# Kernel tuning notes

Hardware: AMD Instinct MI355X
Metric: run time of the kernel (lower is better)

The kernel has to match this reference:

```python
import jax, jax.numpy as jnp
import numpy as np

N_NODES = 100000
N_EDGES = 1600000
IN_C, HID_C, OUT_C, N_CLS = 64, 128, 64, 20


def setup_inputs() -> dict:
    key = jax.random.key(0)
    ks = jax.random.split(key, 8)
    s = lambda k, sh: jax.random.normal(k, sh, dtype=jnp.float32) * (1.0 / np.sqrt(sh[0]))
    return {
        "x": jax.random.normal(ks[0], (N_NODES, IN_C), dtype=jnp.float32),
        "edge_index": jax.random.randint(ks[1], (2, N_EDGES), 0, N_NODES, dtype=jnp.int64),
        "w_self1": s(ks[2], (IN_C, HID_C)),
        "w_neigh1": s(ks[3], (IN_C, HID_C)),
        "b1": jnp.zeros((HID_C,), dtype=jnp.float32),
        "w_self2": s(ks[4], (HID_C, OUT_C)),
        "w_neigh2": s(ks[5], (HID_C, OUT_C)),
        "b2": jnp.zeros((OUT_C,), dtype=jnp.float32),
        "wc": s(ks[6], (OUT_C, N_CLS)),
        "bc": jnp.zeros((N_CLS,), dtype=jnp.float32),
    }


def _sage_mean(feat, src, dst, deg_inv, w_self, w_neigh, b):
    # gather messages along edges, segment-sum at destinations, mean-normalize
    msg_sum = jax.ops.segment_sum(feat[src], dst, num_segments=N_NODES)  # [N, d]
    h_neigh = msg_sum * deg_inv[:, None]
    return feat @ w_self + h_neigh @ w_neigh + b


def reference(x, edge_index, w_self1, w_neigh1, b1, w_self2, w_neigh2, b2, wc, bc):
    src, dst = edge_index[0], edge_index[1]
    deg = jax.ops.segment_sum(jnp.ones((src.shape[0],), dtype=x.dtype), dst,
                              num_segments=N_NODES)
    deg_inv = 1.0 / jnp.maximum(deg, 1.0)  # zero-degree nodes -> 0 neighbor mean
    h = jax.nn.relu(_sage_mean(x, src, dst, deg_inv, w_self1, w_neigh1, b1))
    h = jax.nn.relu(_sage_mean(h, src, dst, deg_inv, w_self2, w_neigh2, b2))
    return h @ wc + bc
```

## Files before the change

### kernel.cpp

```cpp
#include <hip/hip_runtime.h>

#define N_NODES 100000
#define N_EDGES 1600000
#define IN_C    64
#define HID_C   128
#define OUT_C   64
#define N_CLS   20

#define BUCKETS 196
#define XSL     8
#define WCAP    2560
#define EPB     4096
#define CAPB    44

#define EB2       391
#define CVT_BLOCKS 3125
#define NTILES    3125
#define MLP_GRID  512

typedef __attribute__((ext_vector_type(8))) short short8;
typedef __attribute__((ext_vector_type(4))) float floatx4;

__device__ __forceinline__ unsigned short f2bf(float f) {
    union { float f; unsigned u; } v; v.f = f;
    unsigned r = v.u + 0x7FFFu + ((v.u >> 16) & 1u);
    return (unsigned short)(r >> 16);
}
__device__ __forceinline__ unsigned pk2(float lo, float hi) {
    return (unsigned)f2bf(lo) | ((unsigned)f2bf(hi) << 16);
}
__device__ __forceinline__ float bflo(unsigned w) { return __uint_as_float(w << 16); }
__device__ __forceinline__ float bfhi(unsigned w) { return __uint_as_float(w & 0xFFFF0000u); }

#define ACC8(v) do { \
    a0 += bflo((v).x); a1 += bfhi((v).x); a2 += bflo((v).y); a3 += bfhi((v).y); \
    a4 += bflo((v).z); a5 += bfhi((v).z); a6 += bflo((v).w); a7 += bfhi((v).w); } while (0)

__global__ __launch_bounds__(256) void binA_kernel(
        const int* __restrict__ ei, int* __restrict__ bcnt,
        unsigned* __restrict__ bins,
        const float* __restrict__ x, unsigned short* __restrict__ xb,
        const float* __restrict__ ws1, const float* __restrict__ wn1,
        const float* __restrict__ ws2, const float* __restrict__ wn2,
        unsigned short* __restrict__ wt1s, unsigned short* __restrict__ wt1n,
        unsigned short* __restrict__ wt2s, unsigned short* __restrict__ wt2n)
{
    __shared__ unsigned lbins[BUCKETS * CAPB];
    __shared__ unsigned comp[EPB];
    __shared__ unsigned dsti[EPB];
    __shared__ int lcnt[BUCKETS], lofs[BUCKETS], gb[BUCKETS];
    __shared__ int sd[256];

    const int bid = blockIdx.x;
    const int tid = threadIdx.x;

    if (bid >= EB2) {
        if (bid < EB2 + CVT_BLOCKS) {
            int i = (bid - EB2) * 256 + tid;
            float4 a = ((const float4*)x)[(size_t)i * 2];
            float4 b = ((const float4*)x)[(size_t)i * 2 + 1];
            uint4 r;
            r.x = pk2(a.x, a.y); r.y = pk2(a.z, a.w);
            r.z = pk2(b.x, b.y); r.w = pk2(b.z, b.w);
            ((uint4*)xb)[i] = r;
        } else {
            int i = (bid - EB2 - CVT_BLOCKS) * 256 + tid;
            if (i < 8192) {
                int o = i >> 6, c = i & 63;
                wt1s[i] = f2bf(ws1[c * 128 + o]);
                wt1n[i] = f2bf(wn1[c * 128 + o]);
            } else if (i < 16384) {
                int j = i - 8192;
                int o = j >> 7, c = j & 127;
                wt2s[j] = f2bf(ws2[c * 64 + o]);
                wt2n[j] = f2bf(wn2[c * 64 + o]);
            }
        }
        return;
    }

    const int xcd = bid & (XSL - 1);
    const int e0  = bid * EPB;

    for (int w = tid; w < BUCKETS; w += 256) lcnt[w] = 0;
    __syncthreads();

    for (int it = 0; it < EPB / 256; ++it) {
        int e = e0 + it * 256 + tid;
        if (e >= N_EDGES) break;
        int src = ei[e];
        int dst = ei[N_EDGES + e];
        int b = dst >> 9;
        unsigned pk = ((unsigned)(dst & 511) << 17) | (unsigned)src;
        int pos = atomicAdd(&lcnt[b], 1);
        if (pos < CAPB) {
            lbins[b * CAPB + pos] = pk;
        } else {
            int gp = atomicAdd(&bcnt[b * XSL + xcd], 1);
            if (gp < WCAP)
                bins[(unsigned)(b * XSL + xcd) * WCAP + gp] = pk;
        }
    }
    __syncthreads();

    int c = (tid < BUCKETS) ? min(lcnt[tid], CAPB) : 0;
    sd[tid] = c;
    __syncthreads();
    for (int off = 1; off < 256; off <<= 1) {
        int v = 0;
        if (tid >= off) v = sd[tid - off];
        __syncthreads();
        if (tid >= off) sd[tid] += v;
        __syncthreads();
    }
    if (tid < BUCKETS) lofs[tid] = sd[tid] - c;
    __syncthreads();
    const int T = sd[255];

    if (tid < BUCKETS) {
        int cw = min(lcnt[tid], CAPB);
        gb[tid] = (cw > 0) ? atomicAdd(&bcnt[tid * XSL + xcd], cw) : 0;
    }
    __syncthreads();

    if (tid < BUCKETS) {
        int cw = min(lcnt[tid], CAPB);
        int lo = lofs[tid];
        unsigned wb = (unsigned)(tid * XSL + xcd) * WCAP + (unsigned)gb[tid];
        for (int i = 0; i < cw; ++i) {
            comp[lo + i] = lbins[tid * CAPB + i];
            dsti[lo + i] = wb + i;
        }
    }
    __syncthreads();

    for (int i = tid; i < T; i += 256)
        bins[dsti[i]] = comp[i];
}

__global__ __launch_bounds__(256) void buildB_kernel(
        const int* __restrict__ bcnt, const unsigned* __restrict__ bins,
        int* __restrict__ row_ptr, int* __restrict__ sorted_src,
        float* __restrict__ dinv)
{
    __shared__ unsigned ent[16384];
    __shared__ int scnt[XSL], soff[XSL];
    __shared__ int cnt[512], lofs[512], cur[512];
    __shared__ int sd[256];
    __shared__ int gbase_s;

    const int b   = blockIdx.x;
    const int tid = threadIdx.x;
    const int node0 = b * 512;

    int part = 0;
    for (int w = tid; w < b * XSL; w += 256) part += min(bcnt[w], WCAP);
    sd[tid] = part;
    __syncthreads();
    for (int off = 128; off > 0; off >>= 1) {
        if (tid < off) sd[tid] += sd[tid + off];
        __syncthreads();
    }
    if (tid == 0) {
        gbase_s = sd[0];
        if (b == 0) row_ptr[N_NODES] = N_EDGES;
    }
    __syncthreads();

    if (tid < XSL) scnt[tid] = min(bcnt[b * XSL + tid], WCAP);
    { int i = tid; cnt[i] = 0; cnt[i + 256] = 0; }
    __syncthreads();
    if (tid == 0) {
        int acc = 0;
        for (int sl = 0; sl < XSL; ++sl) {
            soff[sl] = acc;
            acc += scnt[sl];
            if (acc > 16384) { scnt[sl] -= (acc - 16384); acc = 16384; }
        }
    }
    __syncthreads();

    for (int sl = 0; sl < XSL; ++sl) {
        int len = scnt[sl];
        const unsigned* seg = bins + (unsigned)(b * XSL + sl) * WCAP;
        int base = soff[sl];
        for (int i = tid; i < len; i += 256) {
            unsigned e = seg[i];
            ent[base + i] = e;
            atomicAdd((unsigned*)&cnt[e >> 17], 1u);
        }
    }
    __syncthreads();
    const int T = soff[XSL - 1] + scnt[XSL - 1];

    int a0 = cnt[2 * tid], a1 = cnt[2 * tid + 1];
    int s2 = a0 + a1;
    sd[tid] = s2;
    __syncthreads();
    for (int off = 1; off < 256; off <<= 1) {
        int v = 0;
        if (tid >= off) v = sd[tid - off];
        __syncthreads();
        if (tid >= off) sd[tid] += v;
        __syncthreads();
    }
    int excl = sd[tid] - s2;
    lofs[2 * tid]     = excl;
    lofs[2 * tid + 1] = excl + a0;
    cur[2 * tid]      = excl;
    cur[2 * tid + 1]  = excl + a0;
    __syncthreads();

    const int gbase = gbase_s;
    for (int j = tid; j < 512; j += 256) {
        int node = node0 + j;
        if (node < N_NODES) {
            row_ptr[node] = gbase + lofs[j];
            dinv[node] = 1.0f / (float)max(cnt[j], 1);
        }
    }
    for (int i = tid; i < T; i += 256) {
        unsigned e = ent[i];
        int dl = e >> 17;
        int p = atomicAdd((unsigned*)&cur[dl], 1u);
        sorted_src[gbase + p] = (int)(e & 0x1FFFFu);
    }
}

__global__ __launch_bounds__(256) void gather1_kernel(
        const int* __restrict__ row_ptr, const int* __restrict__ srcs,
        const unsigned short* __restrict__ featb,
        const float* __restrict__ dinv, unsigned short* __restrict__ aggb)
{
    int gid = blockIdx.x * 256 + threadIdx.x;
    int n = gid >> 3;
    int q = gid & 7;
    const uint4* f4 = (const uint4*)featb;
    float a0=0,a1=0,a2=0,a3=0,a4=0,a5=0,a6=0,a7=0;
    int beg = row_ptr[n];
    int end = row_ptr[n + 1];
    int e = beg;
    for (; e + 4 <= end; e += 4) {
        int s0 = srcs[e], s1 = srcs[e+1], s2 = srcs[e+2], s3 = srcs[e+3];
        uint4 v0 = f4[(size_t)s0 * 8 + q];
        uint4 v1 = f4[(size_t)s1 * 8 + q];
        uint4 v2 = f4[(size_t)s2 * 8 + q];
        uint4 v3 = f4[(size_t)s3 * 8 + q];
        ACC8(v0); ACC8(v1); ACC8(v2); ACC8(v3);
    }
    for (; e < end; ++e) {
        uint4 v = f4[(size_t)srcs[e] * 8 + q];
        ACC8(v);
    }
    float di = dinv[n];
    uint4 r;
    r.x = pk2(a0 * di, a1 * di);
    r.y = pk2(a2 * di, a3 * di);
    r.z = pk2(a4 * di, a5 * di);
    r.w = pk2(a6 * di, a7 * di);
    ((uint4*)aggb)[(size_t)n * 8 + q] = r;
}

__global__ __launch_bounds__(256, 2) void mlp1_kernel(
        const unsigned short* __restrict__ xb,
        const unsigned short* __restrict__ aggb,
        const unsigned short* __restrict__ wt1s,
        const unsigned short* __restrict__ wt1n,
        const float* __restrict__ b1,
        const unsigned short* __restrict__ wt2n,
        const unsigned short* __restrict__ wt2s,
        const float* __restrict__ b2,
        unsigned short* __restrict__ t2b,
        unsigned short* __restrict__ s2b)
{
    __shared__ unsigned short sbuf[32 * 136];

    const int tid  = threadIdx.x;
    const int lane = tid & 63;
    const int wv   = tid >> 6;
    const int quad = lane >> 4;
    const int col  = lane & 15;
    const int nrow = (wv & 1) * 16 + col;
    const int mhalf = wv >> 1;

    short8 wBs0[4], wBs1[4], wBn0[4], wBn1[4];
#pragma unroll
    for (int mt = 0; mt < 4; ++mt) {
        size_t m = (size_t)((mhalf * 4 + mt) * 16 + col);
        wBs0[mt] = *(const short8*)(wt1s + m * 64 +      quad * 8);
        wBs1[mt] = *(const short8*)(wt1s + m * 64 + 32 + quad * 8);
        wBn0[mt] = *(const short8*)(wt1n + m * 64 +      quad * 8);
        wBn1[mt] = *(const short8*)(wt1n + m * 64 + 32 + quad * 8);
    }
    short8 wCt[2][4], wCs[2][4];
#pragma unroll
    for (int mt = 0; mt < 2; ++mt) {
        size_t m = (size_t)((mhalf * 2 + mt) * 16 + col);
#pragma unroll
        for (int kc = 0; kc < 4; ++kc) {
            wCt[mt][kc] = *(const short8*)(wt2n + m * 128 + kc * 32 + quad * 8);
            wCs[mt][kc] = *(const short8*)(wt2s + m * 128 + kc * 32 + quad * 8);
        }
    }
    float4 bv1[4];
#pragma unroll
    for (int mt = 0; mt < 4; ++mt)
        bv1[mt] = *(const float4*)(b1 + (mhalf * 4 + mt) * 16 + quad * 4);
    float4 bv2[2];
#pragma unroll
    for (int mt = 0; mt < 2; ++mt)
        bv2[mt] = *(const float4*)(b2 + (mhalf * 2 + mt) * 16 + quad * 4);

    int tile = blockIdx.x;
    short8 bs0, bs1, bn0, bn1;
    {
        const int nl = tile * 32 + nrow;
        bs0 = *(const short8*)(xb   + (size_t)nl * 64 +      quad * 8);
        bs1 = *(const short8*)(xb   + (size_t)nl * 64 + 32 + quad * 8);
        bn0 = *(const short8*)(aggb + (size_t)nl * 64 +      quad * 8);
        bn1 = *(const short8*)(aggb + (size_t)nl * 64 + 32 + quad * 8);
    }

    while (tile < NTILES) {
        const int nl = tile * 32 + nrow;
        const int next = tile + MLP_GRID;

        floatx4 accB[4];
#pragma unroll
        for (int mt = 0; mt < 4; ++mt) {
            floatx4 acc = {0.f, 0.f, 0.f, 0.f};
            acc = __builtin_amdgcn_mfma_f32_16x16x32_bf16(wBs0[mt], bs0, acc, 0, 0, 0);
            acc = __builtin_amdgcn_mfma_f32_16x16x32_bf16(wBs1[mt], bs1, acc, 0, 0, 0);
            acc = __builtin_amdgcn_mfma_f32_16x16x32_bf16(wBn0[mt], bn0, acc, 0, 0, 0);
            acc = __builtin_amdgcn_mfma_f32_16x16x32_bf16(wBn1[mt], bn1, acc, 0, 0, 0);
            accB[mt] = acc;
        }

        if (next < NTILES) {
            const int nn = next * 32 + nrow;
            bs0 = *(const short8*)(xb   + (size_t)nn * 64 +      quad * 8);
            bs1 = *(const short8*)(xb   + (size_t)nn * 64 + 32 + quad * 8);
            bn0 = *(const short8*)(aggb + (size_t)nn * 64 +      quad * 8);
            bn1 = *(const short8*)(aggb + (size_t)nn * 64 + 32 + quad * 8);
        }

        __syncthreads();
#pragma unroll
        for (int mt = 0; mt < 4; ++mt) {
            int och = (mhalf * 4 + mt) * 16 + quad * 4;
            ushort4 r;
            r.x = f2bf(fmaxf(accB[mt][0] + bv1[mt].x, 0.f));
            r.y = f2bf(fmaxf(accB[mt][1] + bv1[mt].y, 0.f));
            r.z = f2bf(fmaxf(accB[mt][2] + bv1[mt].z, 0.f));
            r.w = f2bf(fmaxf(accB[mt][3] + bv1[mt].w, 0.f));
            *(ushort4*)(sbuf + nrow * 136 + och) = r;
        }
        __syncthreads();

        short8 bfr[4];
#pragma unroll
        for (int kc = 0; kc < 4; ++kc)
            bfr[kc] = *(const short8*)(sbuf + nrow * 136 + kc * 32 + quad * 8);
#pragma unroll
        for (int mt = 0; mt < 2; ++mt) {
            floatx4 at = {0.f, 0.f, 0.f, 0.f};
            floatx4 as = {0.f, 0.f, 0.f, 0.f};
#pragma unroll
            for (int kc = 0; kc < 4; ++kc) {
                at = __builtin_amdgcn_mfma_f32_16x16x32_bf16(wCt[mt][kc], bfr[kc], at, 0, 0, 0);
                as = __builtin_amdgcn_mfma_f32_16x16x32_bf16(wCs[mt][kc], bfr[kc], as, 0, 0, 0);
            }
            int och = (mhalf * 2 + mt) * 16 + quad * 4;
            ushort4 rt;
            rt.x = f2bf(at[0]); rt.y = f2bf(at[1]);
            rt.z = f2bf(at[2]); rt.w = f2bf(at[3]);
            *(ushort4*)(t2b + (size_t)nl * 64 + och) = rt;
            ushort4 rs;
            rs.x = f2bf(as[0] + bv2[mt].x); rs.y = f2bf(as[1] + bv2[mt].y);
            rs.z = f2bf(as[2] + bv2[mt].z); rs.w = f2bf(as[3] + bv2[mt].w);
            *(ushort4*)(s2b + (size_t)nl * 64 + och) = rs;
        }

        tile = next;
    }
}

__global__ __launch_bounds__(256, 8) void fused2_kernel(
        const int* __restrict__ row_ptr, const int* __restrict__ srcs,
        const unsigned short* __restrict__ t2b,
        const unsigned short* __restrict__ s2b,
        const float* __restrict__ dinv,
        const float* __restrict__ wc,
        const float* __restrict__ bc,
        float* __restrict__ out)
{
    __shared__ float hs[32][68];

    const int tid = threadIdx.x;
    const int node0 = blockIdx.x * 32;

    {
        const int q  = tid & 7;
        const int np = tid >> 3;
        const int n = node0 + np;
        const uint4* f4 = (const uint4*)t2b;
        uint4 sv = *(const uint4*)(s2b + (size_t)n * 64 + q * 8);
        float di = dinv[n];
        float a0=0,a1=0,a2=0,a3=0,a4=0,a5=0,a6=0,a7=0;
        int beg = row_ptr[n];
        int end = row_ptr[n + 1];
        int e = beg;
        for (; e + 4 <= end; e += 4) {
            int s0 = srcs[e], s1 = srcs[e+1], s2 = srcs[e+2], s3 = srcs[e+3];
            uint4 v0 = f4[(size_t)s0 * 8 + q];
            uint4 v1 = f4[(size_t)s1 * 8 + q];
            uint4 v2 = f4[(size_t)s2 * 8 + q];
            uint4 v3 = f4[(size_t)s3 * 8 + q];
            ACC8(v0); ACC8(v1); ACC8(v2); ACC8(v3);
        }
        for (; e < end; ++e) {
            uint4 v = f4[(size_t)srcs[e] * 8 + q];
            ACC8(v);
        }
        float* d = hs[np] + q * 8;
        d[0] = fmaxf(a0 * di + bflo(sv.x), 0.f);
        d[1] = fmaxf(a1 * di + bfhi(sv.x), 0.f);
        d[2] = fmaxf(a2 * di + bflo(sv.y), 0.f);
        d[3] = fmaxf(a3 * di + bfhi(sv.y), 0.f);
        d[4] = fmaxf(a4 * di + bflo(sv.z), 0.f);
        d[5] = fmaxf(a5 * di + bfhi(sv.z), 0.f);
        d[6] = fmaxf(a6 * di + bflo(sv.w), 0.f);
        d[7] = fmaxf(a7 * di + bfhi(sv.w), 0.f);
    }
    __syncthreads();

    for (int o = tid; o < 32 * N_CLS; o += 256) {
        int n = o / N_CLS, cls = o % N_CLS;
        float s = bc[cls];
#pragma unroll
        for (int k = 0; k < 64; ++k) s += hs[n][k] * wc[k * N_CLS + cls];
        out[(size_t)(node0 + n) * N_CLS + cls] = s;
    }
}


extern "C" void kernel_launch(void* const* d_in, const int* in_sizes, int n_in,
                              void* d_out, int out_size, void* d_ws, size_t ws_size,
                              hipStream_t stream)
{
    const float* x        = (const float*)d_in[0];
    const int*   ei       = (const int*)  d_in[1];
    const float* w_self1  = (const float*)d_in[2];
    const float* w_neigh1 = (const float*)d_in[3];
    const float* b1       = (const float*)d_in[4];
    const float* w_self2  = (const float*)d_in[5];
    const float* w_neigh2 = (const float*)d_in[6];
    const float* b2       = (const float*)d_in[7];
    const float* wc       = (const float*)d_in[8];
    const float* bc       = (const float*)d_in[9];
    float* out = (float*)d_out;

    const size_t N = N_NODES;
    int*      bcnt    = (int*)d_ws;
    int*      row_ptr = bcnt + BUCKETS * XSL + 8;
    unsigned* bins    = (unsigned*)(row_ptr + N + 8);
    int*      s_src   = (int*)(bins + BUCKETS * XSL * WCAP);
    float*    dinv    = (float*)(s_src + N_EDGES);
    unsigned short* xb    = (unsigned short*)(dinv + N);
    unsigned short* agg1b = xb + 64 * N;
    unsigned short* t2b   = agg1b + 64 * N;
    unsigned short* s2b   = t2b + 64 * N;
    unsigned short* wt1s  = s2b + 64 * N;
    unsigned short* wt1n  = wt1s + 8192;
    unsigned short* wt2s  = wt1n + 8192;
    unsigned short* wt2n  = wt2s + 8192;

    const int BA  = EB2 + CVT_BLOCKS + 64;
    const int GB  = (N_NODES * 8) / 256;
    const int MB32 = (N_NODES + 31) / 32;

    hipMemsetAsync(bcnt, 0, BUCKETS * XSL * sizeof(int), stream);
    binA_kernel<<<BA, 256, 0, stream>>>(ei, bcnt, bins, x, xb,
                                        w_self1, w_neigh1, w_self2, w_neigh2,
                                        wt1s, wt1n, wt2s, wt2n);
    buildB_kernel<<<BUCKETS, 256, 0, stream>>>(bcnt, bins, row_ptr, s_src, dinv);
    gather1_kernel<<<GB, 256, 0, stream>>>(row_ptr, s_src, xb, dinv, agg1b);
    mlp1_kernel<<<MLP_GRID, 256, 0, stream>>>(xb, agg1b, wt1s, wt1n, b1,
                                              wt2n, wt2s, b2, t2b, s2b);
    fused2_kernel<<<MB32, 256, 0, stream>>>(row_ptr, s_src, t2b, s2b, dinv,
                                            wc, bc, out);
}
```

Measured before the change: 263.6 us.

## Halve binning chunk per block, drop LDS compaction, widen buildB to 512 threads

The edge-binning kernel now handles 2048 edges per block across twice as many blocks, with a smaller per-bucket local cap. It drops the comp/dsti staging arrays and instead has each thread binary-search the bucket offset table to write its entry straight to the global bins. The bucket-build kernel moves to 512 threads so each thread owns one destination node, which simplifies the scan and spreads the scatter work. The aim is less LDS use and fewer serial per-bucket loops, for better occupancy and parallelism. In exchange each entry pays a binary search, and the lower local cap pushes more edges to the global atomic overflow path.

```diff
diff --git a/kernel.cpp b/kernel.cpp
--- a/kernel.cpp
+++ b/kernel.cpp
@@ -10,10 +10,10 @@
 #define BUCKETS 196
 #define XSL     8
 #define WCAP    2560
-#define EPB     4096
-#define CAPB    44
-
-#define EB2       391
+#define EPB     2048
+#define CAPB    30
+
+#define EB2       782
 #define CVT_BLOCKS 3125
 #define NTILES    3125
 #define MLP_GRID  512
@@ -46,9 +46,7 @@
         unsigned short* __restrict__ wt2s, unsigned short* __restrict__ wt2n)
 {
     __shared__ unsigned lbins[BUCKETS * CAPB];
-    __shared__ unsigned comp[EPB];
-    __shared__ unsigned dsti[EPB];
-    __shared__ int lcnt[BUCKETS], lofs[BUCKETS], gb[BUCKETS];
+    __shared__ int lcnt[BUCKETS], lofs[BUCKETS + 1], gb[BUCKETS];
     __shared__ int sd[256];
 
     const int bid = blockIdx.x;
@@ -113,32 +111,27 @@
         if (tid >= off) sd[tid] += v;
         __syncthreads();
     }
-    if (tid < BUCKETS) lofs[tid] = sd[tid] - c;
-    __syncthreads();
     const int T = sd[255];
-
     if (tid < BUCKETS) {
-        int cw = min(lcnt[tid], CAPB);
-        gb[tid] = (cw > 0) ? atomicAdd(&bcnt[tid * XSL + xcd], cw) : 0;
-    }
-    __syncthreads();
-
-    if (tid < BUCKETS) {
-        int cw = min(lcnt[tid], CAPB);
-        int lo = lofs[tid];
-        unsigned wb = (unsigned)(tid * XSL + xcd) * WCAP + (unsigned)gb[tid];
-        for (int i = 0; i < cw; ++i) {
-            comp[lo + i] = lbins[tid * CAPB + i];
-            dsti[lo + i] = wb + i;
-        }
-    }
-    __syncthreads();
-
-    for (int i = tid; i < T; i += 256)
-        bins[dsti[i]] = comp[i];
-}
-
-__global__ __launch_bounds__(256) void buildB_kernel(
+        lofs[tid] = sd[tid] - c;
+        gb[tid] = (c > 0) ? atomicAdd(&bcnt[tid * XSL + xcd], c) : 0;
+    }
+    if (tid == 0) lofs[BUCKETS] = T;
+    __syncthreads();
+
+    for (int i = tid; i < T; i += 256) {
+        int lo = 0, hi = BUCKETS;
+        while (hi - lo > 1) {
+            int mid = (lo + hi) >> 1;
+            if (lofs[mid] <= i) lo = mid; else hi = mid;
+        }
+        int off = i - lofs[lo];
+        bins[(unsigned)(lo * XSL + xcd) * WCAP + (unsigned)(gb[lo] + off)] =
+            lbins[lo * CAPB + off];
+    }
+}
+
+__global__ __launch_bounds__(512) void buildB_kernel(
         const int* __restrict__ bcnt, const unsigned* __restrict__ bins,
         int* __restrict__ row_ptr, int* __restrict__ sorted_src,
         float* __restrict__ dinv)
@@ -146,7 +139,7 @@
     __shared__ unsigned ent[16384];
     __shared__ int scnt[XSL], soff[XSL];
     __shared__ int cnt[512], lofs[512], cur[512];
-    __shared__ int sd[256];
+    __shared__ int sd[512];
     __shared__ int gbase_s;
 
     const int b   = blockIdx.x;
@@ -154,10 +147,10 @@
     const int node0 = b * 512;
 
     int part = 0;
-    for (int w = tid; w < b * XSL; w += 256) part += min(bcnt[w], WCAP);
+    for (int w = tid; w < b * XSL; w += 512) part += min(bcnt[w], WCAP);
     sd[tid] = part;
     __syncthreads();
-    for (int off = 128; off > 0; off >>= 1) {
+    for (int off = 256; off > 0; off >>= 1) {
         if (tid < off) sd[tid] += sd[tid + off];
         __syncthreads();
     }
@@ -168,7 +161,7 @@
     __syncthreads();
 
     if (tid < XSL) scnt[tid] = min(bcnt[b * XSL + tid], WCAP);
-    { int i = tid; cnt[i] = 0; cnt[i + 256] = 0; }
+    cnt[tid] = 0;
     __syncthreads();
     if (tid == 0) {
         int acc = 0;
@@ -184,7 +177,7 @@
         int len = scnt[sl];
         const unsigned* seg = bins + (unsigned)(b * XSL + sl) * WCAP;
         int base = soff[sl];
-        for (int i = tid; i < len; i += 256) {
+        for (int i = tid; i < len; i += 512) {
             unsigned e = seg[i];
             ent[base + i] = e;
             atomicAdd((unsigned*)&cnt[e >> 17], 1u);
@@ -193,33 +186,30 @@
     __syncthreads();
     const int T = soff[XSL - 1] + scnt[XSL - 1];
 
-    int a0 = cnt[2 * tid], a1 = cnt[2 * tid + 1];
-    int s2 = a0 + a1;
-    sd[tid] = s2;
-    __syncthreads();
-    for (int off = 1; off < 256; off <<= 1) {
+    const int a = cnt[tid];
+    sd[tid] = a;
+    __syncthreads();
+    for (int off = 1; off < 512; off <<= 1) {
         int v = 0;
         if (tid >= off) v = sd[tid - off];
         __syncthreads();
         if (tid >= off) sd[tid] += v;
         __syncthreads();
     }
-    int excl = sd[tid] - s2;
-    lofs[2 * tid]     = excl;
-    lofs[2 * tid + 1] = excl + a0;
-    cur[2 * tid]      = excl;
-    cur[2 * tid + 1]  = excl + a0;
+    int excl = sd[tid] - a;
+    lofs[tid] = excl;
+    cur[tid]  = excl;
     __syncthreads();
 
     const int gbase = gbase_s;
-    for (int j = tid; j < 512; j += 256) {
-        int node = node0 + j;
+    {
+        int node = node0 + tid;
         if (node < N_NODES) {
-            row_ptr[node] = gbase + lofs[j];
-            dinv[node] = 1.0f / (float)max(cnt[j], 1);
-        }
-    }
-    for (int i = tid; i < T; i += 256) {
+            row_ptr[node] = gbase + lofs[tid];
+            dinv[node] = 1.0f / (float)max(a, 1);
+        }
+    }
+    for (int i = tid; i < T; i += 512) {
         unsigned e = ent[i];
         int dl = e >> 17;
         int p = atomicAdd((unsigned*)&cur[dl], 1u);
@@ -483,7 +473,7 @@
     binA_kernel<<<BA, 256, 0, stream>>>(ei, bcnt, bins, x, xb,
                                         w_self1, w_neigh1, w_self2, w_neigh2,
                                         wt1s, wt1n, wt2s, wt2n);
-    buildB_kernel<<<BUCKETS, 256, 0, stream>>>(bcnt, bins, row_ptr, s_src, dinv);
+    buildB_kernel<<<BUCKETS, 512, 0, stream>>>(bcnt, bins, row_ptr, s_src, dinv);
     gather1_kernel<<<GB, 256, 0, stream>>>(row_ptr, s_src, xb, dinv, agg1b);
     mlp1_kernel<<<MLP_GRID, 256, 0, stream>>>(xb, agg1b, wt1s, wt1n, b1,
                                               wt2n, wt2s, b2, t2b, s2b);
```

Measured after the change: 266.8 us. About the same (+1.2%).
